# Optimization experiments

Measured on AMD Instinct MI355X. Metric: run time of the kernel, lower is better.

## Reference

```python
import jax, jax.numpy as jnp
import numpy as np

B, S, D = 4, 2048, 1024
H, DH = 16, 64  # dim_q = dim_k = D // H
DFF = 4096


def setup_inputs() -> dict:
    key = jax.random.key(0)
    ks = jax.random.split(key, 12)
    sd = 0.02
    x = jax.random.normal(ks[0], (B, S, D), dtype=jnp.float32)
    mask = jax.random.randint(ks[1], (B, S, S), 0, 2) == 1  # True = masked
    Wq = jax.random.normal(ks[2], (H, D, DH), dtype=jnp.float32) * sd
    bq = jnp.zeros((H, DH), dtype=jnp.float32)
    Wk = jax.random.normal(ks[3], (H, D, DH), dtype=jnp.float32) * sd
    bk = jnp.zeros((H, DH), dtype=jnp.float32)
    Wv = jax.random.normal(ks[4], (H, D, DH), dtype=jnp.float32) * sd
    bv = jnp.zeros((H, DH), dtype=jnp.float32)
    Wo = jax.random.normal(ks[5], (H * DH, D), dtype=jnp.float32) * sd
    bo = jnp.zeros((D,), dtype=jnp.float32)
    W1 = jax.random.normal(ks[6], (D, DFF), dtype=jnp.float32) * sd
    b1 = jnp.zeros((DFF,), dtype=jnp.float32)
    W2 = jax.random.normal(ks[7], (DFF, D), dtype=jnp.float32) * sd
    b2 = jnp.zeros((D,), dtype=jnp.float32)
    return dict(x=x, mask=mask, Wq=Wq, bq=bq, Wk=Wk, bk=bk, Wv=Wv, bv=bv,
                Wo=Wo, bo=bo, W1=W1, b1=b1, W2=W2, b2=b2)


def reference(x, mask, Wq, bq, Wk, bk, Wv, bv, Wo, bo, W1, b1, W2, b2):
    # x: [B,S,D]; mask: [B,S,S] bool (True -> masked)
    # Per-head projections, batched over heads: [B,H,S,DH]
    q = jnp.einsum('bsd,hde->bhse', x, Wq) + bq[None, :, None, :]
    k = jnp.einsum('bsd,hde->bhse', x, Wk) + bk[None, :, None, :]
    v = jnp.einsum('bsd,hde->bhse', x, Wv) + bv[None, :, None, :]
    # NOTE: source scales by sqrt(seq_len) (query.size(1)), reproduced faithfully.
    scale = x.shape[1] ** 0.5
    scores = jnp.einsum('bhse,bhte->bhst', q, k) / scale  # [B,H,S,S]
    scores = jnp.where(mask[:, None, :, :], -1e9, scores)
    attn = jax.nn.softmax(scores, axis=-1)
    ctx = jnp.einsum('bhst,bhte->bhse', attn, v)  # [B,H,S,DH]
    # concat heads -> [B,S,H*DH], output projection
    ctx = jnp.transpose(ctx, (0, 2, 1, 3)).reshape(x.shape[0], x.shape[1], -1)
    out = ctx @ Wo + bo
    # FFN (no residual/LayerNorm in source; dropout = identity in eval)
    h = jax.nn.relu(out @ W1 + b1)
    return h @ W2 + b2
```

## Files before the change

### kernel.cpp

```cpp
#include <hip/hip_runtime.h>
#include <hip/hip_bf16.h>


#define SDIM 2048
#define DDIM 1024

using floatx4 = __attribute__((ext_vector_type(4))) float;
using bf16x8  = __attribute__((ext_vector_type(8))) __bf16;
using bf16x4  = __attribute__((ext_vector_type(4))) __bf16;
using short4v = __attribute__((ext_vector_type(4))) short;

#define GLDS16(gptr, lptr)                                                        \
    __builtin_amdgcn_global_load_lds(                                             \
        (const __attribute__((address_space(1))) void*)(uintptr_t)(gptr),         \
        (__attribute__((address_space(3))) void*)(uintptr_t)(lptr), 16, 0, 0)


__global__ void k_f2b(const float* __restrict__ in, __bf16* __restrict__ out) {
    long i = ((long)blockIdx.x * 256 + threadIdx.x) * 4;
    float4 f = *(const float4*)(in + i);
    bf16x4 v;
    v[0] = (__bf16)f.x; v[1] = (__bf16)f.y; v[2] = (__bf16)f.z; v[3] = (__bf16)f.w;
    *(bf16x4*)(out + i) = v;
}

__global__ void k_tr(const float* __restrict__ in, __bf16* __restrict__ out, int R, int C) {
    __shared__ float t[32][33];
    int nrt = R >> 5;
    int tr = blockIdx.x % nrt, tc = blockIdx.x / nrt;
    int r0 = tr * 32, c0 = tc * 32;
    int lx = threadIdx.x & 31, ly = threadIdx.x >> 5;
    #pragma unroll
    for (int i = 0; i < 32; i += 8) t[ly + i][lx] = in[(long)(r0 + ly + i) * C + c0 + lx];
    __syncthreads();
    #pragma unroll
    for (int i = 0; i < 32; i += 8) out[(long)(c0 + ly + i) * R + r0 + lx] = (__bf16)t[lx][ly + i];
}

__global__ void k_pack_qkvw(const float* __restrict__ Wq, const float* __restrict__ Wk,
                            const float* __restrict__ Wv, __bf16* __restrict__ out) {
    int bid = blockIdx.x;
    int dht = bid & 1;
    int dt = (bid >> 1) & 31;
    int h = (bid >> 6) & 15;
    int which = bid >> 10;
    const float* W = (which == 0) ? Wq : (which == 1) ? Wk : Wv;
    __shared__ float t[32][33];
    int lx = threadIdx.x & 31, ly = threadIdx.x >> 5;
    const float* src = W + ((long)h * 1024 + dt * 32) * 64 + dht * 32;
    #pragma unroll
    for (int i = 0; i < 32; i += 8) t[ly + i][lx] = src[(ly + i) * 64 + lx];
    __syncthreads();
    __bf16* dst = out + ((long)(which * 1024 + h * 64 + dht * 32)) * 1024 + dt * 32;
    #pragma unroll
    for (int i = 0; i < 32; i += 8) dst[(long)(ly + i) * 1024 + lx] = (__bf16)t[lx][ly + i];
}

__global__ void k_pack_qkvb(const float* bq, const float* bk, const float* bv, float* out) {
    int i = blockIdx.x * 256 + threadIdx.x;
    if (i < 3072) {
        int which = i >> 10, r = i & 1023;
        const float* s = (which == 0) ? bq : (which == 1) ? bk : bv;
        out[i] = s[r];
    }
}

__global__ void k_probe(const unsigned* __restrict__ m, int* flag) {
    __shared__ int bad;
    if (threadIdx.x == 0) bad = 0;
    __syncthreads();
    int local = 0;
    for (int i = 0; i < 64; i++) {
        unsigned w = m[threadIdx.x + 256 * i];
        if (w != 0u && w != 1u && w != 0x3f800000u) local = 1;
    }
    if (local) atomicOr(&bad, 1);
    __syncthreads();
    if (threadIdx.x == 0) *flag = bad ? 0 : 1;
}

__global__ void k_pack_mask(const void* __restrict__ mask, const int* __restrict__ flag,
                            unsigned long long* __restrict__ bits) {
    long wid = ((long)blockIdx.x * 256 + threadIdx.x) >> 6;
    int lane = threadIdx.x & 63;
    long e = wid * 64 + lane;
    bool pred;
    if (*flag) pred = ((const unsigned*)mask)[e] != 0u;
    else       pred = ((const unsigned char*)mask)[e] != 0;
    unsigned long long bal = __ballot(pred);
    if (lane == 0) bits[wid] = bal;
}

__global__ void k_remap(const unsigned* __restrict__ bitsDW, unsigned* __restrict__ out) {
    int t = blockIdx.x * 256 + threadIdx.x;
    int q = t & 3, kt = (t >> 2) & 15, srow = t >> 6;
    uint4 md = *(const uint4*)(bitsDW + (long)srow * 64 + kt * 4);
    unsigned d[4] = {md.x, md.y, md.z, md.w};
    unsigned acc = 0;
    #pragma unroll
    for (int ct = 0; ct < 8; ct++) {
        unsigned nib = (d[ct >> 1] >> (((ct & 1) << 4) + q * 4)) & 0xFu;
        acc |= nib << (ct * 4);
    }
    out[t] = acc;
}

__global__ void k_trv(const __bf16* __restrict__ Vrow, __bf16* __restrict__ Vt) {
    __shared__ __bf16 t[32][72];
    int p = blockIdx.x >> 6, ts = blockIdx.x & 63;
    int tid = threadIdx.x;
    const __bf16* src = Vrow + ((long)p * 2048 + ts * 32) * 64;
    int s = tid >> 3, c = (tid & 7) * 8;
    *(bf16x8*)&t[s][c] = *(const bf16x8*)&src[s * 64 + c];
    __syncthreads();
    int dh = tid >> 2, sb = (tid & 3) * 8;
    bf16x8 w;
    #pragma unroll
    for (int j = 0; j < 8; j++) w[j] = t[sb + j][dh];
    *(bf16x8*)&Vt[((long)p * 64 + dh) * 2048 + ts * 32 + sb] = w;
}

#define QSZ 8388608L

template <int MODE>
__global__ __launch_bounds__(256, 4) void k_gemm(const __bf16* __restrict__ A,
                                                 const __bf16* __restrict__ Bt,
                                                 const float* __restrict__ bias,
                                                 void* __restrict__ Cout, int Ndim, int K) {
    __shared__ __align__(16) __bf16 As[128 * 64];
    __shared__ __align__(16) __bf16 Bs[128 * 64];
    const int tid = threadIdx.x;
    const int wave = tid >> 6, lane = tid & 63;
    const int q = lane >> 4, l16 = lane & 15;
    const int wr = wave >> 1, wc = wave & 1;
    const long bm = (long)blockIdx.x * 128;
    const long bn = (long)blockIdx.y * 128;
    floatx4 acc[4][4] = {};

    const int srow = lane >> 3;
    const int scol = (((lane & 7) - srow) & 7) * 8;
    const int r8 = l16 & 7;

    const char* apA0 = (const char*)As + (wr * 64 + l16) * 128 + ((q + r8) & 7) * 16;
    const char* apA1 = (const char*)As + (wr * 64 + l16) * 128 + ((q + 4 + r8) & 7) * 16;
    const char* apB0 = (const char*)Bs + (wc * 64 + l16) * 128 + ((q + r8) & 7) * 16;
    const char* apB1 = (const char*)Bs + (wc * 64 + l16) * 128 + ((q + 4 + r8) & 7) * 16;

    for (int k0 = 0; k0 < K; k0 += 64) {
        __syncthreads();
        #pragma unroll
        for (int c = 0; c < 4; c++) {
            int row0 = wave * 32 + c * 8;
            GLDS16(&A[(bm + row0 + srow) * K + k0 + scol], (char*)As + row0 * 128);
            GLDS16(&Bt[(bn + row0 + srow) * K + k0 + scol], (char*)Bs + row0 * 128);
        }
        __syncthreads();
        bf16x8 af[4], bfr[4];
        #pragma unroll
        for (int i = 0; i < 4; i++) af[i] = *(const bf16x8*)(apA0 + i * 2048);
        #pragma unroll
        for (int j = 0; j < 4; j++) bfr[j] = *(const bf16x8*)(apB0 + j * 2048);
        #pragma unroll
        for (int i = 0; i < 4; i++)
            #pragma unroll
            for (int j = 0; j < 4; j++)
                acc[i][j] = __builtin_amdgcn_mfma_f32_16x16x32_bf16(af[i], bfr[j], acc[i][j], 0, 0, 0);
        #pragma unroll
        for (int i = 0; i < 4; i++) af[i] = *(const bf16x8*)(apA1 + i * 2048);
        #pragma unroll
        for (int j = 0; j < 4; j++) bfr[j] = *(const bf16x8*)(apB1 + j * 2048);
        #pragma unroll
        for (int i = 0; i < 4; i++)
            #pragma unroll
            for (int j = 0; j < 4; j++)
                acc[i][j] = __builtin_amdgcn_mfma_f32_16x16x32_bf16(af[i], bfr[j], acc[i][j], 0, 0, 0);
    }

    const int mrow0 = (int)bm + wr * 64 + q * 4;
    const int ncol0 = (int)bn + wc * 64;
    #pragma unroll
    for (int j = 0; j < 4; j++) {
        int nbase = ncol0 + j * 16 + l16;
        float bv = bias[nbase];
        #pragma unroll
        for (int i = 0; i < 4; i++) {
            #pragma unroll
            for (int r = 0; r < 4; r++) {
                int mm = mrow0 + i * 16 + r;
                float v = acc[i][j][r] + bv;
                if (MODE == 2) v = fmaxf(v, 0.f);
                if (MODE == 3) {
                    ((float*)Cout)[(long)mm * Ndim + nbase] = v;
                } else if (MODE == 0) {
                    int which = nbase >> 10, rem = nbase & 1023;
                    int hh = rem >> 6, dh = rem & 63;
                    int bb = mm >> 11, ss = mm & 2047;
                    long pr = (long)(bb * 16 + hh);
                    __bf16* o = (__bf16*)Cout;
                    if (which == 0) {
                        v *= 0.03188152837f;
                        o[(pr * 2048 + ss) * 64 + dh] = (__bf16)v;
                    } else if (which == 1) o[QSZ + (pr * 2048 + ss) * 64 + dh] = (__bf16)v;
                    else o[3 * QSZ + (pr * 2048 + ss) * 64 + dh] = (__bf16)v;
                } else {
                    ((__bf16*)Cout)[(long)mm * Ndim + nbase] = (__bf16)v;
                }
            }
        }
    }
}

__global__ __launch_bounds__(256, 4) void k_attn(const __bf16* __restrict__ Q,
                                                 const __bf16* __restrict__ Kb,
                                                 const __bf16* __restrict__ Vt,
                                                 const unsigned* __restrict__ bitw2,
                                                 __bf16* __restrict__ ctx) {
    __shared__ __align__(16) __bf16 Qs[64 * 64];
    __shared__ __align__(16) __bf16 Ks[128 * 64];
    __shared__ __align__(16) __bf16 Vts[64 * 128];
    const int tid = threadIdx.x, wave = tid >> 6, lane = tid & 63;
    const int q = lane >> 4, l16 = lane & 15;
    const int pair = blockIdx.x & 63, qt = blockIdx.x >> 6;
    const int b = pair >> 4, h = pair & 15;

    const int srow8 = lane >> 3;
    const int scol8 = (((lane & 7) - srow8) & 7) * 8;
    const int r8 = l16 & 7;
    const int vrow = lane >> 4;
    const int vl = lane & 15;

    const __bf16* Qp = Q + ((long)pair * SDIM + qt * 64) * 64;
    #pragma unroll
    for (int c = 0; c < 2; c++) {
        int row0 = wave * 16 + c * 8;
        GLDS16(&Qp[(row0 + srow8) * 64 + scol8], (char*)Qs + row0 * 128);
    }
    __syncthreads();
    const bf16x8 qf0 = *(const bf16x8*)((const char*)Qs + (wave * 16 + l16) * 128 + ((q + r8) & 7) * 16);
    const bf16x8 qf1 = *(const bf16x8*)((const char*)Qs + (wave * 16 + l16) * 128 + ((q + 4 + r8) & 7) * 16);

    const char* kp0 = (const char*)Ks + l16 * 128 + ((q + r8) & 7) * 16;
    const char* kp1 = (const char*)Ks + l16 * 128 + ((q + 4 + r8) & 7) * 16;
    const char* vp[8];
    #pragma unroll
    for (int ct = 0; ct < 8; ct++)
        vp[ct] = (const char*)Vts + l16 * 256 + (q & 1) * 8 + ((ct * 2 + (q >> 1) + l16) & 15) * 16;
    const int qrow = qt * 64 + wave * 16 + l16;
    const unsigned* mp = bitw2 + ((long)(b * SDIM + qrow)) * 64 + q;

    floatx4 o[4] = {};
    floatx4 o5 = {};
    union { unsigned u; short4v s4; float f; } tmp;
    short4v ones;
    { union { unsigned u[2]; short4v s; } c; c.u[0] = 0x3F803F80u; c.u[1] = 0x3F803F80u; ones = c.s; }

    for (int kt = 0; kt < 16; kt++) {
        __syncthreads();
        const __bf16* Kp = Kb + ((long)pair * SDIM + kt * 128) * 64;
        #pragma unroll
        for (int c = 0; c < 4; c++) {
            int row0 = wave * 32 + c * 8;
            GLDS16(&Kp[(row0 + srow8) * 64 + scol8], (char*)Ks + row0 * 128);
        }
        const __bf16* Vp = Vt + ((long)pair * 64) * SDIM + kt * 128;
        #pragma unroll
        for (int c = 0; c < 4; c++) {
            int row0 = wave * 16 + c * 4;
            int gsrc = ((vl - (c * 4 + vrow)) & 15) * 8;
            GLDS16(&Vp[(long)(row0 + vrow) * SDIM + gsrc], (char*)Vts + row0 * 256);
        }
        const unsigned w32 = mp[kt * 4];
        __syncthreads();

        floatx4 st[8];
        #pragma unroll
        for (int ct = 0; ct < 8; ct++) {
            bf16x8 kf0 = *(const bf16x8*)(kp0 + ct * 2048);
            bf16x8 kf1 = *(const bf16x8*)(kp1 + ct * 2048);
            floatx4 z = {};
            z = __builtin_amdgcn_mfma_f32_16x16x32_bf16(kf0, qf0, z, 0, 0, 0);
            z = __builtin_amdgcn_mfma_f32_16x16x32_bf16(kf1, qf1, z, 0, 0, 0);
            st[ct] = z;
        }
        #pragma unroll
        for (int ct = 0; ct < 8; ct++) {
            float p0 = __builtin_amdgcn_exp2f(st[ct][0]);
            float p1 = __builtin_amdgcn_exp2f(st[ct][1]);
            float p2 = __builtin_amdgcn_exp2f(st[ct][2]);
            float p3 = __builtin_amdgcn_exp2f(st[ct][3]);
            p0 = (w32 & (1u << (ct * 4 + 0))) ? 0.f : p0;
            p1 = (w32 & (1u << (ct * 4 + 1))) ? 0.f : p1;
            p2 = (w32 & (1u << (ct * 4 + 2))) ? 0.f : p2;
            p3 = (w32 & (1u << (ct * 4 + 3))) ? 0.f : p3;
            union { float f; unsigned u; } c0, c1, c2, c3;
            c0.f = p0; c1.f = p1; c2.f = p2; c3.f = p3;
            union { unsigned u[2]; short4v s; } pu;
            pu.u[0] = __builtin_amdgcn_perm(c1.u, c0.u, 0x07060302u);
            pu.u[1] = __builtin_amdgcn_perm(c3.u, c2.u, 0x07060302u);
            #pragma unroll
            for (int d = 0; d < 4; d++) {
                union { bf16x4 b; short4v s; } vu;
                vu.b = *(const bf16x4*)(vp[ct] + d * 4096);
                o[d] = __builtin_amdgcn_mfma_f32_16x16x16bf16_1k(vu.s, pu.s, o[d], 0, 0, 0);
            }
            o5 = __builtin_amdgcn_mfma_f32_16x16x16bf16_1k(ones, pu.s, o5, 0, 0, 0);
        }
    }
    float inv = 1.0f / o5[0];
    long base = ((long)b * SDIM + qrow) * DDIM + h * 64;
    #pragma unroll
    for (int d = 0; d < 4; d++) {
        bf16x4 w;
        #pragma unroll
        for (int r = 0; r < 4; r++) w[r] = (__bf16)(o[d][r] * inv);
        *(bf16x4*)&ctx[base + d * 16 + q * 4] = w;
    }
}


extern "C" void kernel_launch(void* const* d_in, const int* in_sizes, int n_in,
                              void* d_out, int out_size, void* d_ws, size_t ws_size,
                              hipStream_t stream) {
    const float* x = (const float*)d_in[0];
    const void* mask = d_in[1];
    const float* Wq = (const float*)d_in[2];
    const float* bq = (const float*)d_in[3];
    const float* Wk = (const float*)d_in[4];
    const float* bk = (const float*)d_in[5];
    const float* Wv = (const float*)d_in[6];
    const float* bv = (const float*)d_in[7];
    const float* Wo = (const float*)d_in[8];
    const float* bo = (const float*)d_in[9];
    const float* W1 = (const float*)d_in[10];
    const float* b1 = (const float*)d_in[11];
    const float* W2 = (const float*)d_in[12];
    const float* b2 = (const float*)d_in[13];

    char* ws = (char*)d_ws;
    __bf16* xb   = (__bf16*)(ws + 0);
    __bf16* Qb   = (__bf16*)(ws + 16777216);
    __bf16* Kb   = (__bf16*)(ws + 33554432);
    __bf16* Vtb  = (__bf16*)(ws + 50331648);
    __bf16* Vrow = (__bf16*)(ws + 67108864);
    __bf16* hbuf = (__bf16*)(ws + 33554432);
    __bf16* wqkvt = (__bf16*)(ws + 100663296);
    __bf16* wot  = (__bf16*)(ws + 106954752);
    __bf16* w1t  = (__bf16*)(ws + 109051904);
    __bf16* w2t  = (__bf16*)(ws + 117440512);
    float* bqkv  = (float*)(ws + 125829120);
    int* flag    = (int*)(ws + 125841408);
    __bf16* ctx = xb;
    __bf16* attn_out = Qb;
    unsigned long long* bits = (unsigned long long*)wqkvt;
    unsigned* bits2 = (unsigned*)((char*)wqkvt + 2097152);
    (void)Vrow;

    k_f2b<<<8192, 256, 0, stream>>>(x, xb);
    k_pack_qkvw<<<3072, 256, 0, stream>>>(Wq, Wk, Wv, wqkvt);
    k_pack_qkvb<<<12, 256, 0, stream>>>(bq, bk, bv, bqkv);
    k_tr<<<1024, 256, 0, stream>>>(Wo, wot, 1024, 1024);
    k_tr<<<4096, 256, 0, stream>>>(W1, w1t, 1024, 4096);
    k_tr<<<4096, 256, 0, stream>>>(W2, w2t, 4096, 1024);
    k_probe<<<1, 256, 0, stream>>>((const unsigned*)mask, flag);

    {
        dim3 g(64, 24);
        k_gemm<0><<<g, 256, 0, stream>>>(xb, wqkvt, bqkv, (void*)Qb, 3072, 1024);
    }
    k_trv<<<4096, 256, 0, stream>>>(Vrow, Vtb);
    k_pack_mask<<<65536, 256, 0, stream>>>(mask, flag, bits);
    k_remap<<<2048, 256, 0, stream>>>((const unsigned*)bits, bits2);
    k_attn<<<2048, 256, 0, stream>>>(Qb, Kb, Vtb, bits2, ctx);
    {
        dim3 g(64, 8);
        k_gemm<1><<<g, 256, 0, stream>>>(ctx, wot, bo, (void*)attn_out, 1024, 1024);
    }
    {
        dim3 g(64, 32);
        k_gemm<2><<<g, 256, 0, stream>>>(attn_out, w1t, b1, (void*)hbuf, 4096, 1024);
    }
    {
        dim3 g(64, 8);
        k_gemm<3><<<g, 256, 0, stream>>>(hbuf, w2t, b2, d_out, 1024, 4096);
    }
}
```

Before: 602.7 us.

## Double query rows per attention block to reuse K/V tiles across two groups

Each attention block now handles 128 query rows instead of 64, with each wave processing two 16-row groups. Every K and V tile loaded into shared memory therefore feeds twice as many MFMAs, halving global K/V traffic and barrier count per query row. The grid is halved and launch bounds relaxed to 3 waves/SIMD to absorb the doubled accumulator and score registers. The MFMA section is wrapped in s_setprio raises. The cost is fewer blocks and lower occupancy.

```diff
diff --git a/kernel.cpp b/kernel.cpp
--- a/kernel.cpp
+++ b/kernel.cpp
@@ -210,12 +210,12 @@
     }
 }
 
-__global__ __launch_bounds__(256, 4) void k_attn(const __bf16* __restrict__ Q,
+__global__ __launch_bounds__(256, 3) void k_attn(const __bf16* __restrict__ Q,
                                                  const __bf16* __restrict__ Kb,
                                                  const __bf16* __restrict__ Vt,
                                                  const unsigned* __restrict__ bitw2,
                                                  __bf16* __restrict__ ctx) {
-    __shared__ __align__(16) __bf16 Qs[64 * 64];
+    __shared__ __align__(16) __bf16 Qs[128 * 64];
     __shared__ __align__(16) __bf16 Ks[128 * 64];
     __shared__ __align__(16) __bf16 Vts[64 * 128];
     const int tid = threadIdx.x, wave = tid >> 6, lane = tid & 63;
@@ -229,15 +229,20 @@
     const int vrow = lane >> 4;
     const int vl = lane & 15;
 
-    const __bf16* Qp = Q + ((long)pair * SDIM + qt * 64) * 64;
-    #pragma unroll
-    for (int c = 0; c < 2; c++) {
-        int row0 = wave * 16 + c * 8;
+    const __bf16* Qp = Q + ((long)pair * SDIM + qt * 128) * 64;
+    #pragma unroll
+    for (int c = 0; c < 4; c++) {
+        int row0 = wave * 32 + c * 8;
         GLDS16(&Qp[(row0 + srow8) * 64 + scol8], (char*)Qs + row0 * 128);
     }
     __syncthreads();
-    const bf16x8 qf0 = *(const bf16x8*)((const char*)Qs + (wave * 16 + l16) * 128 + ((q + r8) & 7) * 16);
-    const bf16x8 qf1 = *(const bf16x8*)((const char*)Qs + (wave * 16 + l16) * 128 + ((q + 4 + r8) & 7) * 16);
+    bf16x8 qf[2][2];
+    #pragma unroll
+    for (int g = 0; g < 2; g++) {
+        const char* qb = (const char*)Qs + (wave * 32 + g * 16 + l16) * 128;
+        qf[g][0] = *(const bf16x8*)(qb + ((q + r8) & 7) * 16);
+        qf[g][1] = *(const bf16x8*)(qb + ((q + 4 + r8) & 7) * 16);
+    }
 
     const char* kp0 = (const char*)Ks + l16 * 128 + ((q + r8) & 7) * 16;
     const char* kp1 = (const char*)Ks + l16 * 128 + ((q + 4 + r8) & 7) * 16;
@@ -245,12 +250,12 @@
     #pragma unroll
     for (int ct = 0; ct < 8; ct++)
         vp[ct] = (const char*)Vts + l16 * 256 + (q & 1) * 8 + ((ct * 2 + (q >> 1) + l16) & 15) * 16;
-    const int qrow = qt * 64 + wave * 16 + l16;
-    const unsigned* mp = bitw2 + ((long)(b * SDIM + qrow)) * 64 + q;
-
-    floatx4 o[4] = {};
-    floatx4 o5 = {};
-    union { unsigned u; short4v s4; float f; } tmp;
+    const int qrow = qt * 128 + wave * 32 + l16;
+    const unsigned* mp0 = bitw2 + ((long)(b * SDIM + qrow)) * 64 + q;
+    const unsigned* mp1 = mp0 + 16 * 64;
+
+    floatx4 o[2][4] = {};
+    floatx4 o5[2] = {};
     short4v ones;
     { union { unsigned u[2]; short4v s; } c; c.u[0] = 0x3F803F80u; c.u[1] = 0x3F803F80u; ones = c.s; }
 
@@ -269,51 +274,77 @@
             int gsrc = ((vl - (c * 4 + vrow)) & 15) * 8;
             GLDS16(&Vp[(long)(row0 + vrow) * SDIM + gsrc], (char*)Vts + row0 * 256);
         }
-        const unsigned w32 = mp[kt * 4];
+        const unsigned w32a = mp0[kt * 4];
+        const unsigned w32b = mp1[kt * 4];
         __syncthreads();
 
-        floatx4 st[8];
+        __builtin_amdgcn_s_setprio(1);
+        floatx4 st0[8], st1[8];
         #pragma unroll
         for (int ct = 0; ct < 8; ct++) {
             bf16x8 kf0 = *(const bf16x8*)(kp0 + ct * 2048);
             bf16x8 kf1 = *(const bf16x8*)(kp1 + ct * 2048);
-            floatx4 z = {};
-            z = __builtin_amdgcn_mfma_f32_16x16x32_bf16(kf0, qf0, z, 0, 0, 0);
-            z = __builtin_amdgcn_mfma_f32_16x16x32_bf16(kf1, qf1, z, 0, 0, 0);
-            st[ct] = z;
+            floatx4 z0 = {}, z1 = {};
+            z0 = __builtin_amdgcn_mfma_f32_16x16x32_bf16(kf0, qf[0][0], z0, 0, 0, 0);
+            z1 = __builtin_amdgcn_mfma_f32_16x16x32_bf16(kf0, qf[1][0], z1, 0, 0, 0);
+            z0 = __builtin_amdgcn_mfma_f32_16x16x32_bf16(kf1, qf[0][1], z0, 0, 0, 0);
+            z1 = __builtin_amdgcn_mfma_f32_16x16x32_bf16(kf1, qf[1][1], z1, 0, 0, 0);
+            st0[ct] = z0; st1[ct] = z1;
         }
         #pragma unroll
         for (int ct = 0; ct < 8; ct++) {
-            float p0 = __builtin_amdgcn_exp2f(st[ct][0]);
-            float p1 = __builtin_amdgcn_exp2f(st[ct][1]);
-            float p2 = __builtin_amdgcn_exp2f(st[ct][2]);
-            float p3 = __builtin_amdgcn_exp2f(st[ct][3]);
-            p0 = (w32 & (1u << (ct * 4 + 0))) ? 0.f : p0;
-            p1 = (w32 & (1u << (ct * 4 + 1))) ? 0.f : p1;
-            p2 = (w32 & (1u << (ct * 4 + 2))) ? 0.f : p2;
-            p3 = (w32 & (1u << (ct * 4 + 3))) ? 0.f : p3;
-            union { float f; unsigned u; } c0, c1, c2, c3;
-            c0.f = p0; c1.f = p1; c2.f = p2; c3.f = p3;
-            union { unsigned u[2]; short4v s; } pu;
-            pu.u[0] = __builtin_amdgcn_perm(c1.u, c0.u, 0x07060302u);
-            pu.u[1] = __builtin_amdgcn_perm(c3.u, c2.u, 0x07060302u);
+            union { unsigned u[2]; short4v s; } pu0, pu1;
+            {
+                float p0 = __builtin_amdgcn_exp2f(st0[ct][0]);
+                float p1 = __builtin_amdgcn_exp2f(st0[ct][1]);
+                float p2 = __builtin_amdgcn_exp2f(st0[ct][2]);
+                float p3 = __builtin_amdgcn_exp2f(st0[ct][3]);
+                p0 = (w32a & (1u << (ct * 4 + 0))) ? 0.f : p0;
+                p1 = (w32a & (1u << (ct * 4 + 1))) ? 0.f : p1;
+                p2 = (w32a & (1u << (ct * 4 + 2))) ? 0.f : p2;
+                p3 = (w32a & (1u << (ct * 4 + 3))) ? 0.f : p3;
+                union { float f; unsigned u; } c0, c1, c2, c3;
+                c0.f = p0; c1.f = p1; c2.f = p2; c3.f = p3;
+                pu0.u[0] = __builtin_amdgcn_perm(c1.u, c0.u, 0x07060302u);
+                pu0.u[1] = __builtin_amdgcn_perm(c3.u, c2.u, 0x07060302u);
+            }
+            {
+                float p0 = __builtin_amdgcn_exp2f(st1[ct][0]);
+                float p1 = __builtin_amdgcn_exp2f(st1[ct][1]);
+                float p2 = __builtin_amdgcn_exp2f(st1[ct][2]);
+                float p3 = __builtin_amdgcn_exp2f(st1[ct][3]);
+                p0 = (w32b & (1u << (ct * 4 + 0))) ? 0.f : p0;
+                p1 = (w32b & (1u << (ct * 4 + 1))) ? 0.f : p1;
+                p2 = (w32b & (1u << (ct * 4 + 2))) ? 0.f : p2;
+                p3 = (w32b & (1u << (ct * 4 + 3))) ? 0.f : p3;
+                union { float f; unsigned u; } c0, c1, c2, c3;
+                c0.f = p0; c1.f = p1; c2.f = p2; c3.f = p3;
+                pu1.u[0] = __builtin_amdgcn_perm(c1.u, c0.u, 0x07060302u);
+                pu1.u[1] = __builtin_amdgcn_perm(c3.u, c2.u, 0x07060302u);
+            }
             #pragma unroll
             for (int d = 0; d < 4; d++) {
                 union { bf16x4 b; short4v s; } vu;
                 vu.b = *(const bf16x4*)(vp[ct] + d * 4096);
-                o[d] = __builtin_amdgcn_mfma_f32_16x16x16bf16_1k(vu.s, pu.s, o[d], 0, 0, 0);
+                o[0][d] = __builtin_amdgcn_mfma_f32_16x16x16bf16_1k(vu.s, pu0.s, o[0][d], 0, 0, 0);
+                o[1][d] = __builtin_amdgcn_mfma_f32_16x16x16bf16_1k(vu.s, pu1.s, o[1][d], 0, 0, 0);
             }
-            o5 = __builtin_amdgcn_mfma_f32_16x16x16bf16_1k(ones, pu.s, o5, 0, 0, 0);
-        }
-    }
-    float inv = 1.0f / o5[0];
-    long base = ((long)b * SDIM + qrow) * DDIM + h * 64;
-    #pragma unroll
-    for (int d = 0; d < 4; d++) {
-        bf16x4 w;
-        #pragma unroll
-        for (int r = 0; r < 4; r++) w[r] = (__bf16)(o[d][r] * inv);
-        *(bf16x4*)&ctx[base + d * 16 + q * 4] = w;
+            o5[0] = __builtin_amdgcn_mfma_f32_16x16x16bf16_1k(ones, pu0.s, o5[0], 0, 0, 0);
+            o5[1] = __builtin_amdgcn_mfma_f32_16x16x16bf16_1k(ones, pu1.s, o5[1], 0, 0, 0);
+        }
+        __builtin_amdgcn_s_setprio(0);
+    }
+    #pragma unroll
+    for (int g = 0; g < 2; g++) {
+        float inv = 1.0f / o5[g][0];
+        long base = ((long)b * SDIM + qrow + g * 16) * DDIM + h * 64;
+        #pragma unroll
+        for (int d = 0; d < 4; d++) {
+            bf16x4 w;
+            #pragma unroll
+            for (int r = 0; r < 4; r++) w[r] = (__bf16)(o[g][d][r] * inv);
+            *(bf16x4*)&ctx[base + d * 16 + q * 4] = w;
+        }
     }
 }
 
@@ -370,7 +401,7 @@
     k_trv<<<4096, 256, 0, stream>>>(Vrow, Vtb);
     k_pack_mask<<<65536, 256, 0, stream>>>(mask, flag, bits);
     k_remap<<<2048, 256, 0, stream>>>((const unsigned*)bits, bits2);
-    k_attn<<<2048, 256, 0, stream>>>(Qb, Kb, Vtb, bits2, ctx);
+    k_attn<<<1024, 256, 0, stream>>>(Qb, Kb, Vtb, bits2, ctx);
     {
         dim3 g(64, 8);
         k_gemm<1><<<g, 256, 0, stream>>>(ctx, wot, bo, (void*)attn_out, 1024, 1024);
```

New measurement: 595.7 us. Within noise of the previous version (-1.2%).
